# Kernel tuning notes

Measured on AMD Instinct MI355X. Metric: run time of the kernel, lower is better.

Reference implementation:

```python
import jax, jax.numpy as jnp
import numpy as np

B = 131072   # number of graphs (ranked lists)
G = 128      # candidates per graph
TEMPERATURE = 1.0

def setup_inputs() -> dict:
    key = jax.random.key(0)
    k1, k2 = jax.random.split(key)
    scores = jax.random.normal(k1, (B * G,), dtype=jnp.float32)
    labels = jax.random.randint(k2, (B * G,), 0, 2, dtype=jnp.int32)  # binary relevance
    batch = jnp.repeat(jnp.arange(B, dtype=jnp.int32), G)             # segment ids, sorted
    return {"scores": scores, "labels": labels, "batch": batch}

def reference(scores, labels, batch):
    # batch encodes B contiguous equal-size segments of length G; reshape replaces
    # the original per-graph Python loop with one vectorized pass.
    s = scores.reshape(B, G) / TEMPERATURE            # [B, G]
    l = labels.reshape(B, G).astype(s.dtype)          # [B, G]
    probs = jax.nn.softmax(s, axis=1)
    pos = jnp.arange(1, G + 1, dtype=s.dtype)
    disc = 1.0 / jnp.log2(pos + 1.0)                  # [G]
    expected_dcg = jnp.sum(probs * l * disc, axis=1)  # [B]
    sorted_l = -jnp.sort(-l, axis=1)                  # descending sort of labels
    idcg = jnp.sum(sorted_l * disc, axis=1)           # [B]
    valid = idcg > 0                                  # graphs with labels.sum()==0 contribute loss 0
    ndcg = expected_dcg / jnp.where(valid, idcg, 1.0)
    loss_g = jnp.where(valid, 1.0 - ndcg, 0.0)
    # original counts every non-NaN graph, including zero-label graphs -> divide by B
    return jnp.sum(loss_g) / B
```

## Files before the change

### kernel.cpp

```cpp
#include <hip/hip_runtime.h>
#include <math.h>


#define G 128

__global__ void build_tables_kernel(float* __restrict__ tabs) {
    int t = threadIdx.x;
    if (t < G) {
        tabs[t] = 1.0f / log2f((float)(t + 2));
    }
    if (t <= G) {
        float s = 0.0f;
        for (int p = 1; p <= t; ++p) s += 1.0f / log2f((float)(p + 1));
        tabs[G + t] = s;
    }
}

__global__ __launch_bounds__(256) void ndcg_main_kernel(
        const float* __restrict__ scores,
        const int*   __restrict__ labels,
        const float* __restrict__ tabs,
        float*       __restrict__ partials) {
    const int lane = threadIdx.x & 63;
    const int li   = lane & 15;
    const int wib  = threadIdx.x >> 6;
    const long long g = (long long)blockIdx.x * 16 + wib * 4 + (lane >> 4);
    const long long base = g * G + li * 8;

    const float4* sp = (const float4*)(scores + base);
    const int4*   lp = (const int4*)(labels + base);
    const float4* dp = (const float4*)(tabs + li * 8);
    float4 sA = sp[0], sB = sp[1];
    int4   lA = lp[0], lB = lp[1];
    float4 dA = dp[0], dB = dp[1];

    float s[8] = {sA.x, sA.y, sA.z, sA.w, sB.x, sB.y, sB.z, sB.w};
    int   l[8] = {lA.x, lA.y, lA.z, lA.w, lB.x, lB.y, lB.z, lB.w};
    float d[8] = {dA.x, dA.y, dA.z, dA.w, dB.x, dB.y, dB.z, dB.w};

    float esum = 0.0f, num = 0.0f;
    int cnt = 0;
#pragma unroll
    for (int j = 0; j < 8; ++j) {
        float e = __expf(s[j]);
        esum += e;
        num  += e * d[j] * (float)l[j];
        cnt  += l[j];
    }

    float cntf = (float)cnt;
#pragma unroll
    for (int m = 1; m <= 8; m <<= 1) {
        esum += __shfl_xor(esum, m, 64);
        num  += __shfl_xor(num,  m, 64);
        cntf += __shfl_xor(cntf, m, 64);
    }
    int c = (int)cntf;
    float idcg = tabs[G + c];
    float loss = (c > 0) ? (1.0f - num / (esum * idcg)) : 0.0f;

    loss += __shfl_xor(loss, 16, 64);
    loss += __shfl_xor(loss, 32, 64);

    __shared__ float wsum[4];
    if (lane == 0) wsum[wib] = loss;
    __syncthreads();
    if (threadIdx.x == 0)
        partials[blockIdx.x] = wsum[0] + wsum[1] + wsum[2] + wsum[3];
}

__global__ void finalize_kernel(const float* __restrict__ partials, int n,
                                float* __restrict__ out, float invB) {
    __shared__ float red[256];
    float a = 0.0f;
    for (int i = threadIdx.x; i < n; i += 256) a += partials[i];
    red[threadIdx.x] = a;
    __syncthreads();
    for (int s = 128; s > 0; s >>= 1) {
        if (threadIdx.x < s) red[threadIdx.x] += red[threadIdx.x + s];
        __syncthreads();
    }
    if (threadIdx.x == 0) out[0] = red[0] * invB;
}

extern "C" void kernel_launch(void* const* d_in, const int* in_sizes, int n_in,
                              void* d_out, int out_size, void* d_ws, size_t ws_size,
                              hipStream_t stream) {
    const float* scores = (const float*)d_in[0];
    const int*   labels = (const int*)d_in[1];

    const int n = in_sizes[0];
    const int B = n / G;
    const int NB = B / 16;

    float* tabs     = (float*)d_ws;
    float* partials = tabs + 512;

    build_tables_kernel<<<1, 256, 0, stream>>>(tabs);
    ndcg_main_kernel<<<NB, 256, 0, stream>>>(scores, labels, tabs, partials);
    finalize_kernel<<<1, 256, 0, stream>>>(partials, NB, (float*)d_out,
                                           1.0f / (float)B);
}
```

Before: 190.0 us.

## Use persistent grid-stride waves with software-prefetched next segment loads

The main kernel now launches a fixed grid of 2048 blocks. Each wave loops over groups of four segments in grid-stride order and issues the loads for the next group before computing the current one. This replaces one-shot blocks (8192 of them) and cuts the partials count the finalize kernel reads. The trade-offs are extra registers for the double buffer and a shared-memory tree reduction per block.

```diff
diff --git a/kernel.cpp b/kernel.cpp
--- a/kernel.cpp
+++ b/kernel.cpp
@@ -20,53 +20,78 @@
         const float* __restrict__ scores,
         const int*   __restrict__ labels,
         const float* __restrict__ tabs,
-        float*       __restrict__ partials) {
+        float*       __restrict__ partials,
+        int nquads) {
     const int lane = threadIdx.x & 63;
     const int li   = lane & 15;
+    const int gs   = lane >> 4;
     const int wib  = threadIdx.x >> 6;
-    const long long g = (long long)blockIdx.x * 16 + wib * 4 + (lane >> 4);
-    const long long base = g * G + li * 8;
+    const int w      = blockIdx.x * 4 + wib;
+    const int nwaves = gridDim.x * 4;
 
-    const float4* sp = (const float4*)(scores + base);
-    const int4*   lp = (const int4*)(labels + base);
     const float4* dp = (const float4*)(tabs + li * 8);
-    float4 sA = sp[0], sB = sp[1];
-    int4   lA = lp[0], lB = lp[1];
     float4 dA = dp[0], dB = dp[1];
+    const float d[8] = {dA.x, dA.y, dA.z, dA.w, dB.x, dB.y, dB.z, dB.w};
 
-    float s[8] = {sA.x, sA.y, sA.z, sA.w, sB.x, sB.y, sB.z, sB.w};
-    int   l[8] = {lA.x, lA.y, lA.z, lA.w, lB.x, lB.y, lB.z, lB.w};
-    float d[8] = {dA.x, dA.y, dA.z, dA.w, dB.x, dB.y, dB.z, dB.w};
+#define LOADQ(SA, SB, LA, LB, Q)                                              \
+    do {                                                                      \
+        const long long base_ = ((long long)(Q) * 4 + gs) * G + li * 8;       \
+        const float4* sp_ = (const float4*)(scores + base_);                  \
+        const int4*   lp_ = (const int4*)(labels + base_);                    \
+        SA = sp_[0]; SB = sp_[1]; LA = lp_[0]; LB = lp_[1];                   \
+    } while (0)
 
-    float esum = 0.0f, num = 0.0f;
-    int cnt = 0;
+    float acc = 0.0f;
+    long long q = w;
+    if (q < nquads) {
+        float4 csA, csB; int4 clA, clB;
+        LOADQ(csA, csB, clA, clB, q);
+        for (;;) {
+            const long long qn = q + nwaves;
+            const bool more = (qn < nquads);
+            float4 nsA, nsB; int4 nlA, nlB;
+            if (more) LOADQ(nsA, nsB, nlA, nlB, qn);
+
+            float s[8] = {csA.x, csA.y, csA.z, csA.w, csB.x, csB.y, csB.z, csB.w};
+            int   l[8] = {clA.x, clA.y, clA.z, clA.w, clB.x, clB.y, clB.z, clB.w};
+
+            float esum = 0.0f, num = 0.0f;
+            int cnt = 0;
 #pragma unroll
-    for (int j = 0; j < 8; ++j) {
-        float e = __expf(s[j]);
-        esum += e;
-        num  += e * d[j] * (float)l[j];
-        cnt  += l[j];
+            for (int j = 0; j < 8; ++j) {
+                float e = __expf(s[j]);
+                esum += e;
+                num  += e * d[j] * (float)l[j];
+                cnt  += l[j];
+            }
+
+            float cntf = (float)cnt;
+#pragma unroll
+            for (int m = 1; m <= 8; m <<= 1) {
+                esum += __shfl_xor(esum, m, 64);
+                num  += __shfl_xor(num,  m, 64);
+                cntf += __shfl_xor(cntf, m, 64);
+            }
+            int c = (int)cntf;
+            float idcg = tabs[G + c];
+            float loss = (c > 0) ? (1.0f - num / (esum * idcg)) : 0.0f;
+            if (li == 0) acc += loss;
+
+            if (!more) break;
+            csA = nsA; csB = nsB; clA = nlA; clB = nlB;
+            q = qn;
+        }
     }
+#undef LOADQ
 
-    float cntf = (float)cnt;
-#pragma unroll
-    for (int m = 1; m <= 8; m <<= 1) {
-        esum += __shfl_xor(esum, m, 64);
-        num  += __shfl_xor(num,  m, 64);
-        cntf += __shfl_xor(cntf, m, 64);
+    __shared__ float red[256];
+    red[threadIdx.x] = acc;
+    __syncthreads();
+    for (int s2 = 128; s2 > 0; s2 >>= 1) {
+        if (threadIdx.x < s2) red[threadIdx.x] += red[threadIdx.x + s2];
+        __syncthreads();
     }
-    int c = (int)cntf;
-    float idcg = tabs[G + c];
-    float loss = (c > 0) ? (1.0f - num / (esum * idcg)) : 0.0f;
-
-    loss += __shfl_xor(loss, 16, 64);
-    loss += __shfl_xor(loss, 32, 64);
-
-    __shared__ float wsum[4];
-    if (lane == 0) wsum[wib] = loss;
-    __syncthreads();
-    if (threadIdx.x == 0)
-        partials[blockIdx.x] = wsum[0] + wsum[1] + wsum[2] + wsum[3];
+    if (threadIdx.x == 0) partials[blockIdx.x] = red[0];
 }
 
 __global__ void finalize_kernel(const float* __restrict__ partials, int n,
@@ -91,13 +116,15 @@
 
     const int n = in_sizes[0];
     const int B = n / G;
-    const int NB = B / 16;
+    const int nquads = B / 4;
 
     float* tabs     = (float*)d_ws;
     float* partials = tabs + 512;
 
+    const int NB = 2048;
+
     build_tables_kernel<<<1, 256, 0, stream>>>(tabs);
-    ndcg_main_kernel<<<NB, 256, 0, stream>>>(scores, labels, tabs, partials);
+    ndcg_main_kernel<<<NB, 256, 0, stream>>>(scores, labels, tabs, partials, nquads);
     finalize_kernel<<<1, 256, 0, stream>>>(partials, NB, (float*)d_out,
                                            1.0f / (float)B);
 }
```

Result: no change. 187.7 us (-1.2%).

## Assign one graph per thread and reduce block losses in shared memory

Applied to the files above, without the earlier changes.

Remaps work so each thread processes an entire 128-element graph with sequential float4 loads, removing the cross-lane shuffle reductions for the softmax sum, numerator and label count. The cumulative ideal-DCG table is staged in shared memory and block partials are reduced with a shared-memory tree. This removes shuffle overhead but makes adjacent threads' loads strided by 512 bytes, which hurts coalescing. It also cuts the grid to far fewer blocks, lowering latency hiding and occupancy.

```diff
diff --git a/kernel.cpp b/kernel.cpp
--- a/kernel.cpp
+++ b/kernel.cpp
@@ -20,53 +20,60 @@
         const float* __restrict__ scores,
         const int*   __restrict__ labels,
         const float* __restrict__ tabs,
-        float*       __restrict__ partials) {
-    const int lane = threadIdx.x & 63;
-    const int li   = lane & 15;
-    const int wib  = threadIdx.x >> 6;
-    const long long g = (long long)blockIdx.x * 16 + wib * 4 + (lane >> 4);
-    const long long base = g * G + li * 8;
+        float*       __restrict__ partials,
+        int B) {
+    const int t = threadIdx.x;
 
-    const float4* sp = (const float4*)(scores + base);
-    const int4*   lp = (const int4*)(labels + base);
-    const float4* dp = (const float4*)(tabs + li * 8);
-    float4 sA = sp[0], sB = sp[1];
-    int4   lA = lp[0], lB = lp[1];
-    float4 dA = dp[0], dB = dp[1];
+    __shared__ float cum_s[G + 1];
+    if (t <= G) cum_s[t] = tabs[G + t];
+    __syncthreads();
 
-    float s[8] = {sA.x, sA.y, sA.z, sA.w, sB.x, sB.y, sB.z, sB.w};
-    int   l[8] = {lA.x, lA.y, lA.z, lA.w, lB.x, lB.y, lB.z, lB.w};
-    float d[8] = {dA.x, dA.y, dA.z, dA.w, dB.x, dB.y, dB.z, dB.w};
+    const int g = blockIdx.x * 256 + t;
+    float loss = 0.0f;
+    if (g < B) {
+        const float4* sp = (const float4*)(scores + (long long)g * G);
+        const int4*   lp = (const int4*)(labels + (long long)g * G);
 
-    float esum = 0.0f, num = 0.0f;
-    int cnt = 0;
+        float4 s[8];
+        int4   l[8];
 #pragma unroll
-    for (int j = 0; j < 8; ++j) {
-        float e = __expf(s[j]);
-        esum += e;
-        num  += e * d[j] * (float)l[j];
-        cnt  += l[j];
+        for (int i = 0; i < 8; ++i) s[i] = sp[i];
+#pragma unroll
+        for (int i = 0; i < 8; ++i) l[i] = lp[i];
+
+        const float4* dv = (const float4*)tabs;
+
+        float es0 = 0.f, es1 = 0.f, es2 = 0.f, es3 = 0.f;
+        float nu0 = 0.f, nu1 = 0.f, nu2 = 0.f, nu3 = 0.f;
+        int cnt = 0;
+#pragma unroll
+        for (int i = 0; i < 8; ++i) {
+            const float4 d = dv[i];
+            const float e0 = __expf(s[i].x);
+            const float e1 = __expf(s[i].y);
+            const float e2 = __expf(s[i].z);
+            const float e3 = __expf(s[i].w);
+            es0 += e0; es1 += e1; es2 += e2; es3 += e3;
+            nu0 += e0 * (l[i].x ? d.x : 0.0f);
+            nu1 += e1 * (l[i].y ? d.y : 0.0f);
+            nu2 += e2 * (l[i].z ? d.z : 0.0f);
+            nu3 += e3 * (l[i].w ? d.w : 0.0f);
+            cnt += l[i].x + l[i].y + l[i].z + l[i].w;
+        }
+        const float esum = (es0 + es1) + (es2 + es3);
+        const float num  = (nu0 + nu1) + (nu2 + nu3);
+        const float idcg = cum_s[cnt];
+        loss = (cnt > 0) ? (1.0f - num / (esum * idcg)) : 0.0f;
     }
 
-    float cntf = (float)cnt;
-#pragma unroll
-    for (int m = 1; m <= 8; m <<= 1) {
-        esum += __shfl_xor(esum, m, 64);
-        num  += __shfl_xor(num,  m, 64);
-        cntf += __shfl_xor(cntf, m, 64);
+    __shared__ float red[256];
+    red[t] = loss;
+    __syncthreads();
+    for (int s2 = 128; s2 > 0; s2 >>= 1) {
+        if (t < s2) red[t] += red[t + s2];
+        __syncthreads();
     }
-    int c = (int)cntf;
-    float idcg = tabs[G + c];
-    float loss = (c > 0) ? (1.0f - num / (esum * idcg)) : 0.0f;
-
-    loss += __shfl_xor(loss, 16, 64);
-    loss += __shfl_xor(loss, 32, 64);
-
-    __shared__ float wsum[4];
-    if (lane == 0) wsum[wib] = loss;
-    __syncthreads();
-    if (threadIdx.x == 0)
-        partials[blockIdx.x] = wsum[0] + wsum[1] + wsum[2] + wsum[3];
+    if (t == 0) partials[blockIdx.x] = red[0];
 }
 
 __global__ void finalize_kernel(const float* __restrict__ partials, int n,
@@ -91,13 +98,13 @@
 
     const int n = in_sizes[0];
     const int B = n / G;
-    const int NB = B / 16;
+    const int NB = (B + 255) / 256;
 
     float* tabs     = (float*)d_ws;
     float* partials = tabs + 512;
 
     build_tables_kernel<<<1, 256, 0, stream>>>(tabs);
-    ndcg_main_kernel<<<NB, 256, 0, stream>>>(scores, labels, tabs, partials);
+    ndcg_main_kernel<<<NB, 256, 0, stream>>>(scores, labels, tabs, partials, B);
     finalize_kernel<<<1, 256, 0, stream>>>(partials, NB, (float*)d_out,
                                            1.0f / (float)B);
 }
```

Result: faster. 168.6 us (-11.3%).

## Drop table-build kernel; compute discount tables in-block with nontemporal loads

Applied to the files above, without the earlier changes.

Removes the separate build_tables launch. Each block now builds the cumulative ideal-DCG table in shared memory with a log-step scan, and each thread recomputes its own discount factors with log2f. Score and label loads become nontemporal vector loads, and the label multiply becomes a select. This saves one kernel launch and the dependent table reads, but every block now pays about 8 barrier-synchronised scan steps plus extra transcendental work.

```diff
diff --git a/kernel.cpp b/kernel.cpp
--- a/kernel.cpp
+++ b/kernel.cpp
@@ -4,47 +4,57 @@
 
 #define G 128
 
-__global__ void build_tables_kernel(float* __restrict__ tabs) {
-    int t = threadIdx.x;
-    if (t < G) {
-        tabs[t] = 1.0f / log2f((float)(t + 2));
-    }
-    if (t <= G) {
-        float s = 0.0f;
-        for (int p = 1; p <= t; ++p) s += 1.0f / log2f((float)(p + 1));
-        tabs[G + t] = s;
-    }
-}
+typedef float f4v __attribute__((ext_vector_type(4)));
+typedef int   i4v __attribute__((ext_vector_type(4)));
 
 __global__ __launch_bounds__(256) void ndcg_main_kernel(
         const float* __restrict__ scores,
         const int*   __restrict__ labels,
-        const float* __restrict__ tabs,
         float*       __restrict__ partials) {
-    const int lane = threadIdx.x & 63;
+    const int t    = threadIdx.x;
+    const int lane = t & 63;
     const int li   = lane & 15;
-    const int wib  = threadIdx.x >> 6;
-    const long long g = (long long)blockIdx.x * 16 + wib * 4 + (lane >> 4);
+    const int wib  = t >> 6;
+    const long long g    = (long long)blockIdx.x * 16 + wib * 4 + (lane >> 4);
     const long long base = g * G + li * 8;
 
-    const float4* sp = (const float4*)(scores + base);
-    const int4*   lp = (const int4*)(labels + base);
-    const float4* dp = (const float4*)(tabs + li * 8);
-    float4 sA = sp[0], sB = sp[1];
-    int4   lA = lp[0], lB = lp[1];
-    float4 dA = dp[0], dB = dp[1];
+    const f4v* sp = (const f4v*)(scores + base);
+    const i4v* lp = (const i4v*)(labels + base);
+    const f4v sA = __builtin_nontemporal_load(sp);
+    const f4v sB = __builtin_nontemporal_load(sp + 1);
+    const i4v lA = __builtin_nontemporal_load(lp);
+    const i4v lB = __builtin_nontemporal_load(lp + 1);
 
-    float s[8] = {sA.x, sA.y, sA.z, sA.w, sB.x, sB.y, sB.z, sB.w};
-    int   l[8] = {lA.x, lA.y, lA.z, lA.w, lB.x, lB.y, lB.z, lB.w};
-    float d[8] = {dA.x, dA.y, dA.z, dA.w, dB.x, dB.y, dB.z, dB.w};
+    __shared__ float cum[G + 1];
+    {
+        if (t <= G) cum[t] = (t == 0) ? 0.0f : 1.0f / log2f((float)(t + 1));
+        __syncthreads();
+#pragma unroll
+        for (int off = 1; off <= G; off <<= 1) {
+            float u = 0.0f;
+            if (t <= G && t >= off) u = cum[t - off];
+            __syncthreads();
+            if (t <= G) cum[t] += u;
+            __syncthreads();
+        }
+    }
+
+    float d[8];
+#pragma unroll
+    for (int j = 0; j < 8; ++j) {
+        d[j] = 1.0f / log2f((float)(li * 8 + j + 2));
+    }
+
+    const float s[8] = {sA[0], sA[1], sA[2], sA[3], sB[0], sB[1], sB[2], sB[3]};
+    const int   l[8] = {lA[0], lA[1], lA[2], lA[3], lB[0], lB[1], lB[2], lB[3]};
 
     float esum = 0.0f, num = 0.0f;
     int cnt = 0;
 #pragma unroll
     for (int j = 0; j < 8; ++j) {
-        float e = __expf(s[j]);
+        const float e = __expf(s[j]);
         esum += e;
-        num  += e * d[j] * (float)l[j];
+        num  += e * (l[j] ? d[j] : 0.0f);
         cnt  += l[j];
     }
 
@@ -55,8 +65,8 @@
         num  += __shfl_xor(num,  m, 64);
         cntf += __shfl_xor(cntf, m, 64);
     }
-    int c = (int)cntf;
-    float idcg = tabs[G + c];
+    const int c = (int)cntf;
+    const float idcg = cum[c];
     float loss = (c > 0) ? (1.0f - num / (esum * idcg)) : 0.0f;
 
     loss += __shfl_xor(loss, 16, 64);
@@ -65,12 +75,13 @@
     __shared__ float wsum[4];
     if (lane == 0) wsum[wib] = loss;
     __syncthreads();
-    if (threadIdx.x == 0)
-        partials[blockIdx.x] = wsum[0] + wsum[1] + wsum[2] + wsum[3];
+    if (t == 0)
+        partials[blockIdx.x] = (wsum[0] + wsum[1]) + (wsum[2] + wsum[3]);
 }
 
-__global__ void finalize_kernel(const float* __restrict__ partials, int n,
-                                float* __restrict__ out, float invB) {
+__global__ __launch_bounds__(256) void finalize_kernel(
+        const float* __restrict__ partials, int n,
+        float* __restrict__ out, float invB) {
     __shared__ float red[256];
     float a = 0.0f;
     for (int i = threadIdx.x; i < n; i += 256) a += partials[i];
@@ -89,15 +100,13 @@
     const float* scores = (const float*)d_in[0];
     const int*   labels = (const int*)d_in[1];
 
-    const int n = in_sizes[0];
-    const int B = n / G;
+    const int n  = in_sizes[0];
+    const int B  = n / G;
     const int NB = B / 16;
 
-    float* tabs     = (float*)d_ws;
-    float* partials = tabs + 512;
+    float* partials = (float*)d_ws;
 
-    build_tables_kernel<<<1, 256, 0, stream>>>(tabs);
-    ndcg_main_kernel<<<NB, 256, 0, stream>>>(scores, labels, tabs, partials);
+    ndcg_main_kernel<<<NB, 256, 0, stream>>>(scores, labels, partials);
     finalize_kernel<<<1, 256, 0, stream>>>(partials, NB, (float*)d_out,
                                            1.0f / (float)B);
 }
```

After: 175.3 us. -7.8%, faster.
